# Performance work log

Measured on AMD Instinct MI355X. Metric: run time of the kernel, lower is better.

The kernel has to match this reference:

```python
import jax, jax.numpy as jnp
import numpy as np

EPS_NORM = 1e-12  # torch F.normalize eps
EPS_PI = 1e-8


def _l2_normalize(x, axis):
    n = jnp.sqrt(jnp.sum(x * x, axis=axis, keepdims=True))
    return x / jnp.maximum(n, EPS_NORM)


def setup_inputs() -> dict:
    key = jax.random.key(0)
    k1, _ = jax.random.split(key)
    B, L, H, E = 8, 1024, 8, 64
    queries = jax.random.normal(k1, (B, L, H, E), dtype=jnp.float32)
    temp = jnp.ones((H, 1), dtype=jnp.float32)  # nn.Parameter(torch.ones(num_heads, 1))
    return {"queries": queries, "temp": temp}


def reference(queries, temp):
    # queries: [B, L, H, E] -> w: [B, H, N, d]
    w = jnp.transpose(queries, (0, 2, 1, 3))
    # normalize over token dim (-2), square, sum over feature dim -> energy [B,H,N]
    w_normed = _l2_normalize(w, axis=-2)
    energy = jnp.sum(w_normed * w_normed, axis=-1)
    # softmax over the HEAD dim (nn.Softmax(dim=1)); temp [H,1] broadcasts over N
    Pi = jax.nn.softmax(energy * temp[None, :, :], axis=1)  # [B,H,N]
    # cosine-similarity attention matrix, mapped to [0,1]
    w_unit = _l2_normalize(w, axis=-1)
    attn_matrix = (jnp.einsum('bhnd,bhmd->bhnm', w_unit, w_unit) + 1.0) * 0.5
    # Pi normalized over tokens
    Pi_norm = Pi / (jnp.sum(Pi, axis=-1, keepdims=True) + EPS_PI)
    # dots: [B,H,1,d] = Pi_norm^T (w**2)
    dots = jnp.einsum('bhn,bhnd->bhd', Pi_norm, w * w)[:, :, None, :]
    attn = 1.0 / (1.0 + dots)  # [B,H,1,d]
    out = -(w * Pi[..., None]) * attn  # [B,H,N,d]
    out = jnp.transpose(out, (0, 2, 1, 3))  # [B,L,H,E]
    attn_reshaped = jnp.transpose(attn_matrix, (0, 2, 1, 3))  # [B,N,H,N]
    return out, attn_reshaped
```

## Files before the change

### kernel.cpp

```cpp
#include <hip/hip_runtime.h>
#include <hip/hip_bf16.h>

#define B_ 8
#define N_ 1024
#define H_ 8
#define D_ 64

typedef __attribute__((ext_vector_type(8))) short short8;
typedef __attribute__((ext_vector_type(4))) float f32x4;

__global__ __launch_bounds__(256) void k_zero(float* __restrict__ p, int n) {
    const int i = blockIdx.x * 256 + threadIdx.x;
    if (i < n) p[i] = 0.f;
}

__global__ __launch_bounds__(256) void k_colsum(const float* __restrict__ q,
                                                ushort* __restrict__ wunit,
                                                float* __restrict__ colsum) {
    const int bh = blockIdx.x, chunk = blockIdx.y;
    const int b = bh >> 3, h = bh & 7;
    const float* qb = q + (size_t)(b * N_ * H_ + h) * D_;
    __shared__ float red[16][64];
    const int t = threadIdx.x;
    const int ng = t >> 4;
    const int dq = (t & 15) * 4;
    float cx = 0.f, cy = 0.f, cz = 0.f, cw = 0.f;
    #pragma unroll
    for (int i = 0; i < 8; ++i) {
        const int n = chunk * 128 + ng + i * 16;
        const float4 v = *(const float4*)(qb + (size_t)n * (H_ * D_) + dq);
        cx += v.x * v.x; cy += v.y * v.y; cz += v.z * v.z; cw += v.w * v.w;
        float ss = v.x * v.x + v.y * v.y + v.z * v.z + v.w * v.w;
        ss += __shfl_xor(ss, 1, 16);
        ss += __shfl_xor(ss, 2, 16);
        ss += __shfl_xor(ss, 4, 16);
        ss += __shfl_xor(ss, 8, 16);
        const float invr = 1.0f / fmaxf(sqrtf(ss), 1e-12f);
        __hip_bfloat162 p0 =
            __float22bfloat162_rn(make_float2(v.x * invr, v.y * invr));
        __hip_bfloat162 p1 =
            __float22bfloat162_rn(make_float2(v.z * invr, v.w * invr));
        uint2 pk;
        pk.x = *(unsigned int*)&p0;
        pk.y = *(unsigned int*)&p1;
        *(uint2*)(wunit + ((size_t)bh * N_ + n) * D_ + dq) = pk;
    }
    red[ng][dq + 0] = cx; red[ng][dq + 1] = cy;
    red[ng][dq + 2] = cz; red[ng][dq + 3] = cw;
    __syncthreads();
    if (t < 64) {
        float s = 0.f;
        #pragma unroll
        for (int i = 0; i < 16; ++i) s += red[i][t];
        atomicAdd(&colsum[bh * 64 + t], s);
    }
}

__global__ __launch_bounds__(256) void k_energy(const float* __restrict__ q,
                                                const float* __restrict__ colsum,
                                                float* __restrict__ energy) {
    const int bh = blockIdx.x, chunk = blockIdx.y;
    const int b = bh >> 3, h = bh & 7;
    __shared__ float inv2[64];
    const int t = threadIdx.x;
    if (t < 64) inv2[t] = 1.0f / fmaxf(colsum[bh * 64 + t], 1e-24f);
    __syncthreads();
    const int n = chunk * 256 + t;
    const float4* row =
        (const float4*)(q + (size_t)(b * N_ * H_ + h) * D_ + (size_t)n * (H_ * D_));
    float e = 0.f;
    #pragma unroll
    for (int i = 0; i < 16; ++i) {
        const float4 v = row[i];
        e += v.x * v.x * inv2[4 * i + 0] + v.y * v.y * inv2[4 * i + 1] +
             v.z * v.z * inv2[4 * i + 2] + v.w * v.w * inv2[4 * i + 3];
    }
    energy[(size_t)bh * N_ + n] = e;
}

__global__ __launch_bounds__(256) void k_pi(const float* __restrict__ energy,
                                            const float* __restrict__ temp,
                                            float* __restrict__ Pi,
                                            float* __restrict__ Pisum) {
    const int idx = blockIdx.x * 256 + threadIdx.x;
    const int b = idx >> 10, n = idx & (N_ - 1);
    float e[H_];
    float m = -1e30f;
    #pragma unroll
    for (int h = 0; h < H_; ++h) {
        e[h] = energy[(size_t)(b * H_ + h) * N_ + n] * temp[h];
        m = fmaxf(m, e[h]);
    }
    float s = 0.f;
    #pragma unroll
    for (int h = 0; h < H_; ++h) { e[h] = expf(e[h] - m); s += e[h]; }
    const float inv = 1.0f / s;
    #pragma unroll
    for (int h = 0; h < H_; ++h) {
        const float p = e[h] * inv;
        Pi[(size_t)(b * H_ + h) * N_ + n] = p;
        float w = p;
        #pragma unroll
        for (int off = 32; off; off >>= 1) w += __shfl_xor(w, off, 64);
        if ((threadIdx.x & 63) == 0) atomicAdd(&Pisum[b * H_ + h], w);
    }
}

__global__ __launch_bounds__(256) void k_dots(const float* __restrict__ q,
                                              const float* __restrict__ Pi,
                                              float* __restrict__ dots) {
    const int bh = blockIdx.x, chunk = blockIdx.y;
    const int b = bh >> 3, h = bh & 7;
    const float* qb = q + (size_t)(b * N_ * H_ + h) * D_;
    const float* Pib = Pi + (size_t)bh * N_;
    __shared__ float red[16][64];
    const int t = threadIdx.x, ng = t >> 4, dq = (t & 15) * 4;
    float cx = 0.f, cy = 0.f, cz = 0.f, cw = 0.f;
    #pragma unroll
    for (int i = 0; i < 8; ++i) {
        const int n = chunk * 128 + ng + i * 16;
        const float p = Pib[n];
        const float4 v = *(const float4*)(qb + (size_t)n * (H_ * D_) + dq);
        cx += p * v.x * v.x; cy += p * v.y * v.y;
        cz += p * v.z * v.z; cw += p * v.w * v.w;
    }
    red[ng][dq + 0] = cx; red[ng][dq + 1] = cy;
    red[ng][dq + 2] = cz; red[ng][dq + 3] = cw;
    __syncthreads();
    if (t < 64) {
        float s = 0.f;
        #pragma unroll
        for (int i = 0; i < 16; ++i) s += red[i][t];
        atomicAdd(&dots[bh * 64 + t], s);
    }
}

__global__ __launch_bounds__(256) void k_attn(const float* __restrict__ dots,
                                              const float* __restrict__ Pisum,
                                              float* __restrict__ attnv) {
    const int i = blockIdx.x * 256 + threadIdx.x;
    const int bh = i >> 6;
    const float invS = 1.0f / (Pisum[bh] + 1e-8f);
    attnv[i] = 1.0f / (1.0f + dots[i] * invS);
}

__global__ __launch_bounds__(256) void k_outw(const float* __restrict__ q,
                                              const float* __restrict__ Pi,
                                              const float* __restrict__ attnv,
                                              float* __restrict__ out0) {
    const int bh = blockIdx.x, chunk = blockIdx.y;
    const int b = bh >> 3, h = bh & 7;
    __shared__ float av[64];
    const int t = threadIdx.x;
    if (t < 64) av[t] = attnv[bh * 64 + t];
    __syncthreads();
    const int n = chunk * 256 + t;
    const float p = -Pi[(size_t)bh * N_ + n];
    const float4* row =
        (const float4*)(q + (size_t)(b * N_ * H_ + h) * D_ + (size_t)n * (H_ * D_));
    float4* orow = (float4*)(out0 + ((size_t)(b * N_ + n) * H_ + h) * D_);
    #pragma unroll
    for (int i = 0; i < 16; ++i) {
        const float4 v = row[i];
        orow[i] = make_float4(v.x * p * av[4 * i + 0], v.y * p * av[4 * i + 1],
                              v.z * p * av[4 * i + 2], v.w * p * av[4 * i + 3]);
    }
}

__global__ __launch_bounds__(256) void k_gram(const ushort* __restrict__ wunit,
                                              float* __restrict__ out1) {
    const int bh = blockIdx.y;
    const int b = bh >> 3, h = bh & 7;
    const int tn = blockIdx.x & 7, tm = blockIdx.x >> 3;
    __shared__ __align__(16) char smem[36864];
    ushort(*lA)[72] = (ushort(*)[72])smem;
    ushort(*lB)[72] = (ushort(*)[72])(smem + 18432);
    float* stg = (float*)smem;
    const int t = threadIdx.x;
    const ushort* Ub = wunit + (size_t)bh * N_ * D_;

    {
        const uint4* gA = (const uint4*)(Ub + (size_t)tn * 128 * D_);
        const uint4* gB = (const uint4*)(Ub + (size_t)tm * 128 * D_);
        #pragma unroll
        for (int c = 0; c < 4; ++c) {
            const int idx = t + c * 256;
            const int row = idx >> 3, col8 = (idx & 7) * 8;
            *(uint4*)&lA[row][col8] = gA[idx];
            *(uint4*)&lB[row][col8] = gB[idx];
        }
    }
    __syncthreads();

    const int wave = t >> 6, lane = t & 63;
    const int rbase = wave * 32;
    const int arow = lane & 15;
    const int kq = (lane >> 4) * 8;

    f32x4 acc[2][8];
    #pragma unroll
    for (int i = 0; i < 2; ++i)
        #pragma unroll
        for (int j = 0; j < 8; ++j) acc[i][j] = (f32x4){0.f, 0.f, 0.f, 0.f};

    #pragma unroll
    for (int kk = 0; kk < 2; ++kk) {
        const int ko = kk * 32 + kq;
        const short8 a0 = *(const short8*)&lA[rbase + arow][ko];
        const short8 a1 = *(const short8*)&lA[rbase + 16 + arow][ko];
        #pragma unroll
        for (int tc = 0; tc < 8; ++tc) {
            const short8 bfr = *(const short8*)&lB[tc * 16 + arow][ko];
            acc[0][tc] = __builtin_amdgcn_mfma_f32_16x16x32_bf16(
                a0, bfr, acc[0][tc], 0, 0, 0);
            acc[1][tc] = __builtin_amdgcn_mfma_f32_16x16x32_bf16(
                a1, bfr, acc[1][tc], 0, 0, 0);
        }
    }
    __syncthreads();

    float* ms = stg + wave * 2112;
    const int col = lane & 15, rq = (lane >> 4) * 4;
    #pragma unroll
    for (int tr = 0; tr < 2; ++tr) {
        #pragma unroll
        for (int tc = 0; tc < 8; ++tc)
            #pragma unroll
            for (int r = 0; r < 4; ++r)
                ms[(rq + r) * 132 + tc * 16 + col] =
                    (acc[tr][tc][r] + 1.0f) * 0.5f;
        #pragma unroll
        for (int i = 0; i < 8; ++i) {
            const int f = i * 64 + lane;
            const int r2 = f >> 5, c2 = f & 31;
            const float4 v = *(const float4*)&ms[r2 * 132 + c2 * 4];
            const int n = tn * 128 + wave * 32 + tr * 16 + r2;
            const int m = tm * 128 + c2 * 4;
            *(float4*)&out1[((size_t)(b * N_ + n) * H_ + h) * N_ + m] = v;
        }
    }
}

extern "C" void kernel_launch(void* const* d_in, const int* in_sizes, int n_in,
                              void* d_out, int out_size, void* d_ws,
                              size_t ws_size, hipStream_t stream) {
    const float* q = (const float*)d_in[0];
    const float* temp = (const float*)d_in[1];
    float* out0 = (float*)d_out;
    float* out1 = out0 + (size_t)B_ * N_ * H_ * D_;

    char* ws = (char*)d_ws;
    ushort* wunit = (ushort*)ws;
    float* Pi     = (float*)(ws + 8388608);
    float* energy = (float*)(ws + 8650752);
    float* colsum = (float*)(ws + 8912896);
    float* dots   = (float*)(ws + 8929280);
    float* Pisum  = (float*)(ws + 8945664);
    float* attnv  = (float*)(ws + 8945920);

    k_zero<<<33, 256, 0, stream>>>(colsum, 8256);
    k_colsum<<<dim3(64, 8), 256, 0, stream>>>(q, wunit, colsum);
    k_energy<<<dim3(64, 4), 256, 0, stream>>>(q, colsum, energy);
    k_pi<<<32, 256, 0, stream>>>(energy, temp, Pi, Pisum);
    k_dots<<<dim3(64, 8), 256, 0, stream>>>(q, Pi, dots);
    k_attn<<<16, 256, 0, stream>>>(dots, Pisum, attnv);
    k_outw<<<dim3(64, 4), 256, 0, stream>>>(q, Pi, attnv, out0);
    k_gram<<<dim3(64, 64), 256, 0, stream>>>(wunit, out1);
}
```

Before: 334.2 us.

## Fuse energy, softmax and dots kernels; replace global atomics with partial sums

```diff
diff --git a/kernel.cpp b/kernel.cpp
--- a/kernel.cpp
+++ b/kernel.cpp
@@ -9,14 +9,9 @@
 typedef __attribute__((ext_vector_type(8))) short short8;
 typedef __attribute__((ext_vector_type(4))) float f32x4;
 
-__global__ __launch_bounds__(256) void k_zero(float* __restrict__ p, int n) {
-    const int i = blockIdx.x * 256 + threadIdx.x;
-    if (i < n) p[i] = 0.f;
-}
-
 __global__ __launch_bounds__(256) void k_colsum(const float* __restrict__ q,
                                                 ushort* __restrict__ wunit,
-                                                float* __restrict__ colsum) {
+                                                float* __restrict__ cpart) {
     const int bh = blockIdx.x, chunk = blockIdx.y;
     const int b = bh >> 3, h = bh & 7;
     const float* qb = q + (size_t)(b * N_ * H_ + h) * D_;
@@ -52,118 +47,102 @@
         float s = 0.f;
         #pragma unroll
         for (int i = 0; i < 16; ++i) s += red[i][t];
-        atomicAdd(&colsum[bh * 64 + t], s);
-    }
-}
-
-__global__ __launch_bounds__(256) void k_energy(const float* __restrict__ q,
-                                                const float* __restrict__ colsum,
-                                                float* __restrict__ energy) {
-    const int bh = blockIdx.x, chunk = blockIdx.y;
+        cpart[((size_t)chunk * 64 + bh) * 64 + t] = s;
+    }
+}
+
+__global__ __launch_bounds__(256) void k_epi(const float* __restrict__ q,
+                                             const float* __restrict__ cpart,
+                                             const float* __restrict__ temp,
+                                             float* __restrict__ Pi,
+                                             float* __restrict__ dpart,
+                                             float* __restrict__ ppart) {
+    const int b = blockIdx.x >> 5, chunk = blockIdx.x & 31;
+    const int n0 = chunk * 32;
+    const int t = threadIdx.x;
+    const int n_l = t >> 3, h = t & 7;
+    __shared__ float inv2[8][66];
+    __shared__ float dres[8][64];
+    __shared__ float psum[8];
+    #pragma unroll
+    for (int r = 0; r < 2; ++r) {
+        const int idx = r * 256 + t, hh = idx >> 6, d = idx & 63;
+        float s = 0.f;
+        #pragma unroll
+        for (int c = 0; c < 8; ++c)
+            s += cpart[((size_t)c * 64 + b * 8 + hh) * 64 + d];
+        inv2[hh][d] = 1.0f / fmaxf(s, 1e-24f);
+        dres[hh][d] = 0.f;
+    }
+    if (t < 8) psum[t] = 0.f;
+    __syncthreads();
+    const float* row = q + ((size_t)(b * N_ + n0 + n_l) * H_ + h) * D_;
+    float4 s2[16];
+    float e = 0.f;
+    #pragma unroll
+    for (int i = 0; i < 16; ++i) {
+        const float4 v = ((const float4*)row)[i];
+        s2[i] = make_float4(v.x * v.x, v.y * v.y, v.z * v.z, v.w * v.w);
+        e += s2[i].x * inv2[h][4 * i + 0] + s2[i].y * inv2[h][4 * i + 1] +
+             s2[i].z * inv2[h][4 * i + 2] + s2[i].w * inv2[h][4 * i + 3];
+    }
+    e *= temp[h];
+    float m = e;
+    m = fmaxf(m, __shfl_xor(m, 1, 8));
+    m = fmaxf(m, __shfl_xor(m, 2, 8));
+    m = fmaxf(m, __shfl_xor(m, 4, 8));
+    const float ex = expf(e - m);
+    float ssum = ex;
+    ssum += __shfl_xor(ssum, 1, 8);
+    ssum += __shfl_xor(ssum, 2, 8);
+    ssum += __shfl_xor(ssum, 4, 8);
+    const float p = ex / ssum;
+    Pi[(size_t)(b * 8 + h) * N_ + n0 + n_l] = p;
+    atomicAdd(&psum[h], p);
+    #pragma unroll
+    for (int i = 0; i < 16; ++i) {
+        atomicAdd(&dres[h][4 * i + 0], p * s2[i].x);
+        atomicAdd(&dres[h][4 * i + 1], p * s2[i].y);
+        atomicAdd(&dres[h][4 * i + 2], p * s2[i].z);
+        atomicAdd(&dres[h][4 * i + 3], p * s2[i].w);
+    }
+    __syncthreads();
+    const size_t base = (size_t)(b * 32 + chunk) * 512;
+    dpart[base + t] = ((const float*)dres)[t];
+    dpart[base + 256 + t] = ((const float*)dres)[256 + t];
+    if (t < 8) ppart[(size_t)(b * 32 + chunk) * 8 + t] = psum[t];
+}
+
+__global__ __launch_bounds__(256) void k_out2(const float* __restrict__ q,
+                                              const float* __restrict__ Pi,
+                                              const float* __restrict__ dpart,
+                                              const float* __restrict__ ppart,
+                                              float* __restrict__ out0) {
+    const int bh = blockIdx.x, nc = blockIdx.y;
     const int b = bh >> 3, h = bh & 7;
-    __shared__ float inv2[64];
-    const int t = threadIdx.x;
-    if (t < 64) inv2[t] = 1.0f / fmaxf(colsum[bh * 64 + t], 1e-24f);
-    __syncthreads();
-    const int n = chunk * 256 + t;
+    __shared__ float av[64];
+    const int t = threadIdx.x;
+    if (t < 64) {
+        float ds = 0.f, S = 0.f;
+        #pragma unroll
+        for (int c = 0; c < 32; ++c) {
+            ds += dpart[((size_t)(b * 32 + c) * 8 + h) * 64 + t];
+            S += ppart[(size_t)(b * 32 + c) * 8 + h];
+        }
+        av[t] = 1.0f / (1.0f + ds / (S + 1e-8f));
+    }
+    __syncthreads();
+    const int n = nc * 256 + t;
+    const float p = -Pi[(size_t)bh * N_ + n];
     const float4* row =
-        (const float4*)(q + (size_t)(b * N_ * H_ + h) * D_ + (size_t)n * (H_ * D_));
-    float e = 0.f;
+        (const float4*)(q + ((size_t)(b * N_ + n) * H_ + h) * D_);
+    f32x4* orow = (f32x4*)(out0 + ((size_t)(b * N_ + n) * H_ + h) * D_);
     #pragma unroll
     for (int i = 0; i < 16; ++i) {
         const float4 v = row[i];
-        e += v.x * v.x * inv2[4 * i + 0] + v.y * v.y * inv2[4 * i + 1] +
-             v.z * v.z * inv2[4 * i + 2] + v.w * v.w * inv2[4 * i + 3];
-    }
-    energy[(size_t)bh * N_ + n] = e;
-}
-
-__global__ __launch_bounds__(256) void k_pi(const float* __restrict__ energy,
-                                            const float* __restrict__ temp,
-                                            float* __restrict__ Pi,
-                                            float* __restrict__ Pisum) {
-    const int idx = blockIdx.x * 256 + threadIdx.x;
-    const int b = idx >> 10, n = idx & (N_ - 1);
-    float e[H_];
-    float m = -1e30f;
-    #pragma unroll
-    for (int h = 0; h < H_; ++h) {
-        e[h] = energy[(size_t)(b * H_ + h) * N_ + n] * temp[h];
-        m = fmaxf(m, e[h]);
-    }
-    float s = 0.f;
-    #pragma unroll
-    for (int h = 0; h < H_; ++h) { e[h] = expf(e[h] - m); s += e[h]; }
-    const float inv = 1.0f / s;
-    #pragma unroll
-    for (int h = 0; h < H_; ++h) {
-        const float p = e[h] * inv;
-        Pi[(size_t)(b * H_ + h) * N_ + n] = p;
-        float w = p;
-        #pragma unroll
-        for (int off = 32; off; off >>= 1) w += __shfl_xor(w, off, 64);
-        if ((threadIdx.x & 63) == 0) atomicAdd(&Pisum[b * H_ + h], w);
-    }
-}
-
-__global__ __launch_bounds__(256) void k_dots(const float* __restrict__ q,
-                                              const float* __restrict__ Pi,
-                                              float* __restrict__ dots) {
-    const int bh = blockIdx.x, chunk = blockIdx.y;
-    const int b = bh >> 3, h = bh & 7;
-    const float* qb = q + (size_t)(b * N_ * H_ + h) * D_;
-    const float* Pib = Pi + (size_t)bh * N_;
-    __shared__ float red[16][64];
-    const int t = threadIdx.x, ng = t >> 4, dq = (t & 15) * 4;
-    float cx = 0.f, cy = 0.f, cz = 0.f, cw = 0.f;
-    #pragma unroll
-    for (int i = 0; i < 8; ++i) {
-        const int n = chunk * 128 + ng + i * 16;
-        const float p = Pib[n];
-        const float4 v = *(const float4*)(qb + (size_t)n * (H_ * D_) + dq);
-        cx += p * v.x * v.x; cy += p * v.y * v.y;
-        cz += p * v.z * v.z; cw += p * v.w * v.w;
-    }
-    red[ng][dq + 0] = cx; red[ng][dq + 1] = cy;
-    red[ng][dq + 2] = cz; red[ng][dq + 3] = cw;
-    __syncthreads();
-    if (t < 64) {
-        float s = 0.f;
-        #pragma unroll
-        for (int i = 0; i < 16; ++i) s += red[i][t];
-        atomicAdd(&dots[bh * 64 + t], s);
-    }
-}
-
-__global__ __launch_bounds__(256) void k_attn(const float* __restrict__ dots,
-                                              const float* __restrict__ Pisum,
-                                              float* __restrict__ attnv) {
-    const int i = blockIdx.x * 256 + threadIdx.x;
-    const int bh = i >> 6;
-    const float invS = 1.0f / (Pisum[bh] + 1e-8f);
-    attnv[i] = 1.0f / (1.0f + dots[i] * invS);
-}
-
-__global__ __launch_bounds__(256) void k_outw(const float* __restrict__ q,
-                                              const float* __restrict__ Pi,
-                                              const float* __restrict__ attnv,
-                                              float* __restrict__ out0) {
-    const int bh = blockIdx.x, chunk = blockIdx.y;
-    const int b = bh >> 3, h = bh & 7;
-    __shared__ float av[64];
-    const int t = threadIdx.x;
-    if (t < 64) av[t] = attnv[bh * 64 + t];
-    __syncthreads();
-    const int n = chunk * 256 + t;
-    const float p = -Pi[(size_t)bh * N_ + n];
-    const float4* row =
-        (const float4*)(q + (size_t)(b * N_ * H_ + h) * D_ + (size_t)n * (H_ * D_));
-    float4* orow = (float4*)(out0 + ((size_t)(b * N_ + n) * H_ + h) * D_);
-    #pragma unroll
-    for (int i = 0; i < 16; ++i) {
-        const float4 v = row[i];
-        orow[i] = make_float4(v.x * p * av[4 * i + 0], v.y * p * av[4 * i + 1],
-                              v.z * p * av[4 * i + 2], v.w * p * av[4 * i + 3]);
+        f32x4 o = {v.x * p * av[4 * i + 0], v.y * p * av[4 * i + 1],
+                   v.z * p * av[4 * i + 2], v.w * p * av[4 * i + 3]};
+        __builtin_nontemporal_store(o, orow + i);
     }
 }
 
@@ -171,7 +150,7 @@
                                               float* __restrict__ out1) {
     const int bh = blockIdx.y;
     const int b = bh >> 3, h = bh & 7;
-    const int tn = blockIdx.x & 7, tm = blockIdx.x >> 3;
+    const int tm = blockIdx.x & 7, tn = blockIdx.x >> 3;
     __shared__ __align__(16) char smem[36864];
     ushort(*lA)[72] = (ushort(*)[72])smem;
     ushort(*lB)[72] = (ushort(*)[72])(smem + 18432);
@@ -252,18 +231,12 @@
     char* ws = (char*)d_ws;
     ushort* wunit = (ushort*)ws;
     float* Pi     = (float*)(ws + 8388608);
-    float* energy = (float*)(ws + 8650752);
-    float* colsum = (float*)(ws + 8912896);
-    float* dots   = (float*)(ws + 8929280);
-    float* Pisum  = (float*)(ws + 8945664);
-    float* attnv  = (float*)(ws + 8945920);
-
-    k_zero<<<33, 256, 0, stream>>>(colsum, 8256);
-    k_colsum<<<dim3(64, 8), 256, 0, stream>>>(q, wunit, colsum);
-    k_energy<<<dim3(64, 4), 256, 0, stream>>>(q, colsum, energy);
-    k_pi<<<32, 256, 0, stream>>>(energy, temp, Pi, Pisum);
-    k_dots<<<dim3(64, 8), 256, 0, stream>>>(q, Pi, dots);
-    k_attn<<<16, 256, 0, stream>>>(dots, Pisum, attnv);
-    k_outw<<<dim3(64, 4), 256, 0, stream>>>(q, Pi, attnv, out0);
+    float* cpart  = (float*)(ws + 8650752);
+    float* dpart  = (float*)(ws + 8781824);
+    float* ppart  = (float*)(ws + 9306112);
+
+    k_colsum<<<dim3(64, 8), 256, 0, stream>>>(q, wunit, cpart);
+    k_epi<<<256, 256, 0, stream>>>(q, cpart, temp, Pi, dpart, ppart);
+    k_out2<<<dim3(64, 4), 256, 0, stream>>>(q, Pi, dpart, ppart, out0);
     k_gram<<<dim3(64, 64), 256, 0, stream>>>(wunit, out1);
 }
```

After: 361.6 us. 8.2% more time.
